# Kernel tuning notes

Hardware: AMD Instinct MI355X
Metric: run time of the kernel (lower is better)

The kernel has to match this reference:

```python
import jax, jax.numpy as jnp
import numpy as np

B, S, HID, NH, NKV, HD, PS = 4, 1024, 4096, 32, 8, 128, 16
PPS = S // PS            # pages per sequence
NP = B * PPS             # total pages
NNZ = B * S


def _llama31_freqs(head_dim):
    # flashinfer apply_llama31_rope defaults: theta=5e5, scale=8, low=1, high=4, old_ctx=8192
    half = head_dim // 2
    theta, scale, low_ff, high_ff, old_ctx = 500000.0, 8.0, 1.0, 4.0, 8192.0
    freq = 1.0 / (theta ** (jnp.arange(half, dtype=jnp.float32) * 2.0 / head_dim))
    wavelen = 2.0 * jnp.pi / freq
    low_wl, high_wl = old_ctx / low_ff, old_ctx / high_ff
    smooth = (old_ctx / wavelen - low_ff) / (high_ff - low_ff)
    return jnp.where(wavelen < high_wl, freq,
                     jnp.where(wavelen > low_wl, freq / scale,
                               (1.0 - smooth) * freq / scale + smooth * freq))


def _rope(x, pos, freqs):
    # x: [nnz, H, D], non-interleaved (rotate-half) layout
    ang = pos.astype(jnp.float32)[:, None] * freqs[None, :]          # [nnz, D/2]
    cos, sin = jnp.cos(ang)[:, None, :], jnp.sin(ang)[:, None, :]    # [nnz, 1, D/2]
    x1, x2 = jnp.split(x, 2, axis=-1)
    return jnp.concatenate([x1 * cos - x2 * sin, x2 * cos + x1 * sin], axis=-1)


def setup_inputs() -> dict:
    key = jax.random.key(0)
    ks = jax.random.split(key, 6)
    std = 0.02
    return {
        "hidden_states": jax.random.normal(ks[0], (NNZ, HID), jnp.float32),
        "wq": jax.random.normal(ks[1], (NH * HD, HID), jnp.float32) * std,
        "wk": jax.random.normal(ks[2], (NKV * HD, HID), jnp.float32) * std,
        "wv": jax.random.normal(ks[3], (NKV * HD, HID), jnp.float32) * std,
        "wo": jax.random.normal(ks[4], (HID, NH * HD), jnp.float32) * std,
        "kv_cache": jnp.zeros((1, NP, 2, PS, NKV, HD), jnp.float32),
        "position_ids": jnp.tile(jnp.arange(S, dtype=jnp.int32), B),
        "kv_page_indices": jnp.arange(NP, dtype=jnp.int32),
        "kv_page_indptr": jnp.arange(B + 1, dtype=jnp.int32) * PPS,
        "kv_last_page_lens": jnp.full((B,), PS, jnp.int32),
        "qo_indptr": jnp.arange(B + 1, dtype=jnp.int32) * S,
    }


def reference(hidden_states, wq, wk, wv, wo, kv_cache, position_ids,
              kv_page_indices, kv_page_indptr, kv_last_page_lens, qo_indptr):
    nnz = hidden_states.shape[0]
    b = qo_indptr.shape[0] - 1
    s = nnz // b
    # fused QKV projections (nn.Linear stores [out, in])
    q = (hidden_states @ wq.T).reshape(nnz, NH, HD)
    k = (hidden_states @ wk.T).reshape(nnz, NKV, HD)
    v = (hidden_states @ wv.T).reshape(nnz, NKV, HD)
    # inline Llama-3.1 RoPE with per-token position ids
    freqs = _llama31_freqs(HD)
    q = _rope(q, position_ids, freqs)
    k = _rope(k, position_ids, freqs)
    # paged-KV append: scatter k/v into pages at (page_id, slot)
    cache = kv_cache[0]                                   # [NP, 2, PS, NKV, HD]
    ps = cache.shape[2]
    pages = kv_page_indices.reshape(b, -1)                # [B, PPS]
    bidx = jnp.repeat(jnp.arange(b), s)
    pid = pages[bidx, position_ids // ps]
    slot = position_ids % ps
    cache = cache.at[pid, 0, slot].set(k).at[pid, 1, slot].set(v)
    # paged attention: gather per-sequence K/V from pages, causal SDPA with GQA
    flat = pages.reshape(-1)
    kf = cache[flat, 0].reshape(b, s, NKV, HD)
    vf = cache[flat, 1].reshape(b, s, NKV, HD)
    g = NH // NKV
    kr = jnp.repeat(kf, g, axis=2)                        # [B, S, NH, HD]
    vr = jnp.repeat(vf, g, axis=2)
    qb = q.reshape(b, s, NH, HD)
    scale = 1.0 / jnp.sqrt(jnp.float32(HD))
    scores = jnp.einsum('bqhd,bkhd->bhqk', qb, kr) * scale
    mask = jnp.tril(jnp.ones((s, s), bool))
    scores = jnp.where(mask[None, None], scores, jnp.float32(-1e30))
    attn = jax.nn.softmax(scores, axis=-1)
    out = jnp.einsum('bhqk,bkhd->bqhd', attn, vr).reshape(nnz, NH * HD)
    return out @ wo.T
```

## Files before the change

### kernel.cpp

```cpp
#include <hip/hip_runtime.h>

typedef unsigned short u16;
typedef __bf16 bf16x8 __attribute__((ext_vector_type(8)));
typedef float f32x4 __attribute__((ext_vector_type(4)));

__device__ __forceinline__ u16 f2bf(float f) {
  unsigned int u = __float_as_uint(f);
  u += 0x7fffu + ((u >> 16) & 1u);
  return (u16)(u >> 16);
}
__device__ __forceinline__ float bf2f(u16 v) {
  return __uint_as_float(((unsigned int)v) << 16);
}

__device__ __forceinline__ void gl_lds16(const u16* g, u16* l) {
  auto* lp = reinterpret_cast<__attribute__((address_space(3))) unsigned int*>(
      reinterpret_cast<uintptr_t>(l));
  auto* gp = reinterpret_cast<const __attribute__((address_space(1))) unsigned int*>(
      reinterpret_cast<uintptr_t>(g));
  __builtin_amdgcn_global_load_lds(gp, lp, 16, 0, 0);
}

__global__ __launch_bounds__(256) void cvt_kernel(const float* __restrict__ in,
                                                  u16* __restrict__ out, int n4) {
  int i = blockIdx.x * 256 + threadIdx.x;
  if (i >= n4) return;
  float4 v = ((const float4*)in)[i];
  ushort4 o;
  o.x = f2bf(v.x); o.y = f2bf(v.y); o.z = f2bf(v.z); o.w = f2bf(v.w);
  ((ushort4*)out)[i] = o;
}


#define BARRIER() __builtin_amdgcn_s_barrier()
#define VMCNT(n_) asm volatile("s_waitcnt vmcnt(" #n_ ")" ::: "memory")
#define PH_SYNC()                                           \
  do {                                                      \
    BARRIER();                                              \
    asm volatile("s_waitcnt lgkmcnt(0)" ::: "memory");      \
    __builtin_amdgcn_sched_barrier(0);                      \
  } while (0)

#define STAGE_A(b_, h_, kt_)                                                        \
  gl_lds16(gA + (size_t)((h_) * 128) * K + (size_t)(kt_) * 32,                      \
           lds + (b_) * 16384 + (h_) * 4096 + w * 512)

#define STAGE_B(b_, h_, kt_)                                                        \
  gl_lds16(gB + (size_t)((h_) * 128) * K + (size_t)(kt_) * 32,                      \
           lds + (b_) * 16384 + 8192 + (h_) * 4096 + w * 512)

#define LOADS_A(b_, qm_)                                                            \
  do {                                                                              \
    _Pragma("unroll") for (int i2 = 0; i2 < 4; i2++)                                \
      ar[i2] = *(const bf16x8*)&lds[(b_) * 16384 + arow + ((qm_)*4 + i2) * 512 + ax]; \
  } while (0)

#define LOADS_B(b_, qn_)                                                            \
  do {                                                                              \
    _Pragma("unroll") for (int j2 = 0; j2 < 2; j2++)                                \
      br[(qn_)*2 + j2] =                                                            \
          *(const bf16x8*)&lds[(b_) * 16384 + brow + ((qn_)*2 + j2) * 512 + ax];    \
  } while (0)

#define MFMA_Q(qm_, qn_)                                                            \
  do {                                                                              \
    __builtin_amdgcn_s_setprio(1);                                                  \
    _Pragma("unroll") for (int i2 = 0; i2 < 4; i2++) {                              \
      _Pragma("unroll") for (int j2 = 0; j2 < 2; j2++) {                            \
        acc[(qm_)*4 + i2][(qn_)*2 + j2] = __builtin_amdgcn_mfma_f32_16x16x32_bf16(  \
            ar[i2], br[(qn_)*2 + j2], acc[(qm_)*4 + i2][(qn_)*2 + j2], 0, 0, 0);    \
      }                                                                             \
    }                                                                               \
    __builtin_amdgcn_s_setprio(0);                                                  \
  } while (0)

template <int OUT_BF16>
__global__ __launch_bounds__(512, 2) void gemm8p(const u16* __restrict__ A,
                                                 const u16* __restrict__ B,
                                                 void* __restrict__ Cv,
                                                 int M, int N, int K) {
  __shared__ u16 lds[32768];
  (void)M;
  const int t = threadIdx.x, lane = t & 63, w = t >> 6;
  const int col = lane & 15, quad = lane >> 4;
  const int wm = w >> 2, wn = w & 3;

  const int nwg = gridDim.x * gridDim.y;
  const int wgid = blockIdx.y * gridDim.x + blockIdx.x;
  const int xcd = wgid & 7, lin = wgid >> 3;
  const int q8 = nwg >> 3, r8 = nwg & 7;
  const int nid = (xcd < r8 ? xcd * (q8 + 1) : r8 * (q8 + 1) + (xcd - r8) * q8) + lin;
  const int m0 = (nid / gridDim.x) * 256;
  const int n0 = (nid % gridDim.x) * 256;

  const int pr_ = t >> 3;
  const int s_ = (t & 7) ^ (pr_ & 7);
  const int srow = (pr_ << 1) | (s_ >> 2);
  const int sj = s_ & 3;
  const u16* gA = A + (size_t)(m0 + srow) * K + sj * 8;
  const u16* gB = B + (size_t)(n0 + srow) * K + sj * 8;

  const int arow = wm * 4096;
  const int brow = 8192 + wn * 2048;
  const int ax = (col >> 1) * 64 +
                 (((((col & 1) << 2) | quad) ^ (col >> 1)) << 3);

  f32x4 acc[8][4] = {};
  bf16x8 ar[4], br[4];

  STAGE_A(0, 0, 0); STAGE_A(0, 1, 0);
  STAGE_B(0, 0, 0); STAGE_B(0, 1, 0);
  STAGE_B(1, 0, 1); STAGE_B(1, 1, 1);
  VMCNT(2);
  BARRIER();

  const int NIT = K >> 6;
  for (int it = 0; it < NIT - 1; ++it) {
    const int kt = it * 2;
    LOADS_A(0, 0); LOADS_B(0, 0);
    STAGE_A(1, 0, kt + 1);
    PH_SYNC(); MFMA_Q(0, 0); BARRIER();
    LOADS_B(0, 1);
    STAGE_A(1, 1, kt + 1);
    PH_SYNC(); MFMA_Q(0, 1); BARRIER();
    LOADS_A(0, 1);
    STAGE_B(0, 0, kt + 2);
    PH_SYNC(); MFMA_Q(1, 0); BARRIER();
    STAGE_B(0, 1, kt + 2);
    PH_SYNC(); MFMA_Q(1, 1); VMCNT(2); BARRIER();
    LOADS_A(1, 0); LOADS_B(1, 0);
    STAGE_A(0, 0, kt + 2);
    PH_SYNC(); MFMA_Q(0, 0); BARRIER();
    LOADS_B(1, 1);
    STAGE_A(0, 1, kt + 2);
    PH_SYNC(); MFMA_Q(0, 1); BARRIER();
    LOADS_A(1, 1);
    STAGE_B(1, 0, kt + 3);
    PH_SYNC(); MFMA_Q(1, 0); BARRIER();
    STAGE_B(1, 1, kt + 3);
    PH_SYNC(); MFMA_Q(1, 1); VMCNT(2); BARRIER();
  }

  {
    const int kl = 2 * NIT - 1;
    LOADS_A(0, 0); LOADS_B(0, 0);
    STAGE_A(1, 0, kl);
    PH_SYNC(); MFMA_Q(0, 0); BARRIER();
    LOADS_B(0, 1);
    STAGE_A(1, 1, kl);
    PH_SYNC(); MFMA_Q(0, 1); BARRIER();
    LOADS_A(0, 1);
    PH_SYNC(); MFMA_Q(1, 0); BARRIER();
    PH_SYNC(); MFMA_Q(1, 1); VMCNT(0); BARRIER();
    LOADS_A(1, 0); LOADS_B(1, 0);
    PH_SYNC(); MFMA_Q(0, 0); BARRIER();
    LOADS_B(1, 1);
    PH_SYNC(); MFMA_Q(0, 1); BARRIER();
    LOADS_A(1, 1);
    PH_SYNC(); MFMA_Q(1, 0); BARRIER();
    MFMA_Q(1, 1);
  }

#pragma unroll
  for (int i = 0; i < 8; i++) {
#pragma unroll
    for (int j = 0; j < 4; j++) {
      const int mb = m0 + wm * 128 + i * 16 + quad * 4;
      const int n = n0 + wn * 64 + j * 16 + col;
#pragma unroll
      for (int r = 0; r < 4; r++) {
        float v = acc[i][j][r];
        if constexpr (OUT_BF16)
          ((u16*)Cv)[(size_t)(mb + r) * N + n] = f2bf(v);
        else
          ((float*)Cv)[(size_t)(mb + r) * N + n] = v;
      }
    }
  }
}

__global__ __launch_bounds__(256) void transpose_kernel(const u16* __restrict__ in,
                                                        u16* __restrict__ out,
                                                        int in_stride, int out_stride) {
  __shared__ u16 tile[64][72];
  const int t = threadIdx.x;
  const int bm = blockIdx.y;
  const int bn = blockIdx.x;
  const int r = t >> 3, c = (t & 7) * 8;
  const u16* src = in + (size_t)(bm * 64 + r) * in_stride + bn * 64 + c;
  *(uint4*)&tile[r][c] = *(const uint4*)src;
  *(uint4*)&tile[r + 32][c] = *(const uint4*)(src + (size_t)32 * in_stride);
  __syncthreads();
  u16 vals[8];
  u16* dst = out + (size_t)(bn * 64 + r) * out_stride + bm * 64 + c;
#pragma unroll
  for (int i = 0; i < 8; i++) vals[i] = tile[c + i][r];
  *(uint4*)dst = *(uint4*)vals;
#pragma unroll
  for (int i = 0; i < 8; i++) vals[i] = tile[c + i][r + 32];
  *(uint4*)(dst + (size_t)32 * out_stride) = *(uint4*)vals;
}

__global__ __launch_bounds__(256) void rope_kernel(u16* __restrict__ X,
                                                   const int* __restrict__ pos_ids,
                                                   int log2H, int row_stride) {
  int tid = blockIdx.x * 256 + threadIdx.x;
  int i = tid & 63;
  int rest = tid >> 6;
  int h = rest & ((1 << log2H) - 1);
  int token = rest >> log2H;
  float pos = (float)pos_ids[token];
  float fr = __builtin_exp2f(-(float)i * (18.93156856932417f / 64.0f));
  float wl = 6.283185307179586f / fr;
  float f2;
  if (wl < 2048.0f) f2 = fr;
  else if (wl > 8192.0f) f2 = fr * 0.125f;
  else {
    float sm = (8192.0f / wl - 1.0f) * (1.0f / 3.0f);
    f2 = (1.0f - sm) * fr * 0.125f + sm * fr;
  }
  float ang = pos * f2;
  float ss = sinf(ang), cc = cosf(ang);
  size_t base = (size_t)token * row_stride + (size_t)h * 128 + i;
  float x1 = bf2f(X[base]), x2 = bf2f(X[base + 64]);
  X[base] = f2bf(x1 * cc - x2 * ss);
  X[base + 64] = f2bf(x2 * cc + x1 * ss);
}

__global__ __launch_bounds__(256) void attn_kernel(const u16* __restrict__ Qg,
                                                   const u16* __restrict__ Kg,
                                                   const u16* __restrict__ VTg,
                                                   u16* __restrict__ Og,
                                                   int QS, int KS) {
  const int qt = 15 - blockIdx.x;
  const int h = blockIdx.y, b = blockIdx.z;
  const int kvh = h >> 2;
  const int t = threadIdx.x, lane = t & 63, w = t >> 6;
  const int col = lane & 15, quad = lane >> 4;

  __shared__ u16 Ks[2][64 * 128];
  __shared__ u16 Vt[2][128 * 64];
  __shared__ u16 Ps[4][16][72];

  const u16* Kbase = Kg + (size_t)(b * 1024) * KS + kvh * 128;
  const u16* Vbase = VTg + (size_t)(kvh * 128) * 4096 + b * 1024;

  auto stage_kv = [&](int bb, int j) {
#pragma unroll
    for (int c = 0; c < 4; c++) {
      int ch = w * 4 + c;
      int krow = ch * 4 + (lane >> 4);
      int kg = (lane & 15) ^ (krow & 15);
      gl_lds16(Kbase + (size_t)(j * 64 + krow) * KS + kg * 8, &Ks[bb][ch * 512]);
      int vrow = ch * 8 + (lane >> 3);
      int vg = (lane & 7) ^ (vrow & 7);
      gl_lds16(Vbase + (size_t)vrow * 4096 + j * 64 + vg * 8, &Vt[bb][ch * 512]);
    }
  };

  {
    const u16* Qbase = Qg + (size_t)(b * 1024 + qt * 64) * QS + h * 128;
#pragma unroll
    for (int c = 0; c < 4; c++) {
      int ch = w * 4 + c;
      int row = ch * 4 + (lane >> 4);
      int g = (lane & 15) ^ (row & 15);
      gl_lds16(Qbase + (size_t)row * QS + g * 8, &Ks[0][ch * 512]);
    }
  }
  stage_kv(1, 0);
  __syncthreads();
  bf16x8 qa[4];
#pragma unroll
  for (int kk = 0; kk < 4; kk++) {
    int row = w * 16 + col;
    qa[kk] = *(const bf16x8*)&Ks[0][row * 128 + (((quad + 4 * kk) ^ col) << 3)];
  }
  BARRIER();

  f32x4 o[8] = {};
  float m_i[4] = {-3.0e38f, -3.0e38f, -3.0e38f, -3.0e38f};
  float l_i[4] = {};

  const float cf = 0.08838834764831845f * 1.4426950408889634f;
  const int qrow0 = qt * 64 + w * 16 + quad * 4;

  for (int j = 0; j <= qt; j++) {
    const int bb = (j + 1) & 1;
    if (j < qt) {
      stage_kv(bb ^ 1, j + 1);
      VMCNT(8);
    } else {
      VMCNT(0);
    }
    BARRIER();

    const u16* Ksb = &Ks[bb][0];
    const u16* Vtb = &Vt[bb][0];

    f32x4 s[4] = {};
    __builtin_amdgcn_s_setprio(1);
#pragma unroll
    for (int nb = 0; nb < 4; nb++) {
      int key = nb * 16 + col;
#pragma unroll
      for (int kk = 0; kk < 4; kk++) {
        bf16x8 kb2 = *(const bf16x8*)&Ksb[key * 128 + (((quad + 4 * kk) ^ col) << 3)];
        s[nb] = __builtin_amdgcn_mfma_f32_16x16x32_bf16(qa[kk], kb2, s[nb], 0, 0, 0);
      }
    }
    __builtin_amdgcn_s_setprio(0);

    if (j == qt) {
#pragma unroll
      for (int nb = 0; nb < 4; nb++)
#pragma unroll
        for (int rr = 0; rr < 4; rr++)
          if (j * 64 + nb * 16 + col > qrow0 + rr) s[nb][rr] = -3.0e38f;
    }

    float mnew[4];
#pragma unroll
    for (int rr = 0; rr < 4; rr++) {
      mnew[rr] = m_i[rr];
#pragma unroll
      for (int nb = 0; nb < 4; nb++) mnew[rr] = fmaxf(mnew[rr], s[nb][rr]);
    }
#pragma unroll
    for (int off = 1; off < 16; off <<= 1)
#pragma unroll
      for (int rr = 0; rr < 4; rr++)
        mnew[rr] = fmaxf(mnew[rr], __shfl_xor(mnew[rr], off));

    float p[4][4], rs[4], alpha[4];
#pragma unroll
    for (int rr = 0; rr < 4; rr++) {
      alpha[rr] = __builtin_exp2f((m_i[rr] - mnew[rr]) * cf);
      m_i[rr] = mnew[rr];
      rs[rr] = 0.0f;
    }
#pragma unroll
    for (int nb = 0; nb < 4; nb++)
#pragma unroll
      for (int rr = 0; rr < 4; rr++) {
        p[nb][rr] = __builtin_exp2f((s[nb][rr] - mnew[rr]) * cf);
        rs[rr] += p[nb][rr];
      }
#pragma unroll
    for (int off = 1; off < 16; off <<= 1)
#pragma unroll
      for (int rr = 0; rr < 4; rr++) rs[rr] += __shfl_xor(rs[rr], off);
#pragma unroll
    for (int rr = 0; rr < 4; rr++) l_i[rr] = l_i[rr] * alpha[rr] + rs[rr];
#pragma unroll
    for (int nb2 = 0; nb2 < 8; nb2++)
#pragma unroll
      for (int rr = 0; rr < 4; rr++) o[nb2][rr] *= alpha[rr];

#pragma unroll
    for (int nb = 0; nb < 4; nb++)
#pragma unroll
      for (int rr = 0; rr < 4; rr++)
        Ps[w][quad * 4 + rr][nb * 16 + col] = f2bf(p[nb][rr]);

    bf16x8 pa0 = *(const bf16x8*)&Ps[w][col][quad * 8];
    bf16x8 pa1 = *(const bf16x8*)&Ps[w][col][quad * 8 + 32];
    __builtin_amdgcn_s_setprio(1);
#pragma unroll
    for (int nb2 = 0; nb2 < 8; nb2++) {
      int d = nb2 * 16 + col;
      bf16x8 vb0 = *(const bf16x8*)&Vtb[d * 64 + ((quad ^ (col & 7)) << 3)];
      bf16x8 vb1 = *(const bf16x8*)&Vtb[d * 64 + ((((quad + 4) & 7) ^ (col & 7)) << 3)];
      o[nb2] = __builtin_amdgcn_mfma_f32_16x16x32_bf16(pa0, vb0, o[nb2], 0, 0, 0);
      o[nb2] = __builtin_amdgcn_mfma_f32_16x16x32_bf16(pa1, vb1, o[nb2], 0, 0, 0);
    }
    __builtin_amdgcn_s_setprio(0);

    BARRIER();
  }

  float inv[4];
#pragma unroll
  for (int rr = 0; rr < 4; rr++) inv[rr] = 1.0f / l_i[rr];
#pragma unroll
  for (int nb2 = 0; nb2 < 8; nb2++)
#pragma unroll
    for (int rr = 0; rr < 4; rr++) {
      size_t off2 = (size_t)(b * 1024 + qt * 64 + w * 16 + quad * 4 + rr) * 4096 +
                    h * 128 + nb2 * 16 + col;
      Og[off2] = f2bf(o[nb2][rr] * inv[rr]);
    }
}

extern "C" void kernel_launch(void* const* d_in, const int* in_sizes, int n_in,
                              void* d_out, int out_size, void* d_ws, size_t ws_size,
                              hipStream_t stream) {
  const float* hs = (const float*)d_in[0];
  const float* wq = (const float*)d_in[1];
  const float* wk = (const float*)d_in[2];
  const float* wv = (const float*)d_in[3];
  const float* wo = (const float*)d_in[4];
  const int* pos = (const int*)d_in[6];
  float* out = (float*)d_out;

  char* ws = (char*)d_ws;
  const size_t MB = 1ull << 20;
  u16* hs_bf   = (u16*)(ws + 0);
  u16* wqkv_bf = (u16*)(ws + 32 * MB);
  u16* QKV     = (u16*)(ws + 80 * MB);
  u16* wo_bf = (u16*)(ws + 0);
  u16* AOb   = (u16*)(ws + 32 * MB);
  u16* VTb   = (u16*)(ws + 64 * MB);

  cvt_kernel<<<16384, 256, 0, stream>>>(hs, hs_bf, 4194304);
  cvt_kernel<<<16384, 256, 0, stream>>>(wq, wqkv_bf, 4194304);
  cvt_kernel<<<4096, 256, 0, stream>>>(wk, wqkv_bf + 16777216, 1048576);
  cvt_kernel<<<4096, 256, 0, stream>>>(wv, wqkv_bf + 20971520, 1048576);

  gemm8p<1><<<dim3(24, 16), 512, 0, stream>>>(hs_bf, wqkv_bf, QKV, 4096, 6144, 4096);

  rope_kernel<<<32768, 256, 0, stream>>>(QKV, pos, 5, 6144);
  rope_kernel<<<8192, 256, 0, stream>>>(QKV + 4096, pos, 3, 6144);

  transpose_kernel<<<dim3(16, 64), 256, 0, stream>>>(QKV + 5120, VTb, 6144, 4096);

  cvt_kernel<<<16384, 256, 0, stream>>>(wo, wo_bf, 4194304);

  attn_kernel<<<dim3(16, 32, 4), 256, 0, stream>>>(QKV, QKV + 4096, VTb, AOb, 6144, 6144);

  gemm8p<0><<<dim3(16, 16), 512, 0, stream>>>(AOb, wo_bf, out, 4096, 4096, 4096);
}
```

Before: 801.4 us.

## Process two adjacent query tiles per attention block to reuse staged K/V

Each attention workgroup now handles two consecutive 64-row query tiles, with a separate set of accumulators for each. Every K/V tile staged into LDS is used by both query tiles, which halves K/V global loads and the number of workgroups. The causal mask is now applied on every iteration instead of only the diagonal tile. Holding two sets of accumulators raises register pressure, and launch_bounds(256,2) is added to cap it; fewer workgroups may also lower parallelism and load balance.

```diff
diff --git a/kernel.cpp b/kernel.cpp
--- a/kernel.cpp
+++ b/kernel.cpp
@@ -227,12 +227,13 @@
   X[base + 64] = f2bf(x2 * cc + x1 * ss);
 }
 
-__global__ __launch_bounds__(256) void attn_kernel(const u16* __restrict__ Qg,
-                                                   const u16* __restrict__ Kg,
-                                                   const u16* __restrict__ VTg,
-                                                   u16* __restrict__ Og,
-                                                   int QS, int KS) {
-  const int qt = 15 - blockIdx.x;
+__global__ __launch_bounds__(256, 2) void attn_kernel(const u16* __restrict__ Qg,
+                                                      const u16* __restrict__ Kg,
+                                                      const u16* __restrict__ VTg,
+                                                      u16* __restrict__ Og,
+                                                      int QS, int KS) {
+  const int qtp = 7 - blockIdx.x;
+  const int qA = qtp * 2, qB = qA + 1;
   const int h = blockIdx.y, b = blockIdx.z;
   const int kvh = h >> 2;
   const int t = threadIdx.x, lane = t & 63, w = t >> 6;
@@ -259,45 +260,40 @@
   };
 
   {
-    const u16* Qbase = Qg + (size_t)(b * 1024 + qt * 64) * QS + h * 128;
+    const u16* QbA = Qg + (size_t)(b * 1024 + qA * 64) * QS + h * 128;
+    const u16* QbB = Qg + (size_t)(b * 1024 + qB * 64) * QS + h * 128;
 #pragma unroll
     for (int c = 0; c < 4; c++) {
       int ch = w * 4 + c;
       int row = ch * 4 + (lane >> 4);
       int g = (lane & 15) ^ (row & 15);
-      gl_lds16(Qbase + (size_t)row * QS + g * 8, &Ks[0][ch * 512]);
+      gl_lds16(QbA + (size_t)row * QS + g * 8, &Ks[0][ch * 512]);
+      gl_lds16(QbB + (size_t)row * QS + g * 8, &Vt[0][ch * 512]);
     }
   }
   stage_kv(1, 0);
   __syncthreads();
-  bf16x8 qa[4];
+  bf16x8 qaA[4], qaB[4];
 #pragma unroll
   for (int kk = 0; kk < 4; kk++) {
     int row = w * 16 + col;
-    qa[kk] = *(const bf16x8*)&Ks[0][row * 128 + (((quad + 4 * kk) ^ col) << 3)];
+    int off = row * 128 + (((quad + 4 * kk) ^ col) << 3);
+    qaA[kk] = *(const bf16x8*)&Ks[0][off];
+    qaB[kk] = *(const bf16x8*)&Vt[0][off];
   }
   BARRIER();
 
-  f32x4 o[8] = {};
-  float m_i[4] = {-3.0e38f, -3.0e38f, -3.0e38f, -3.0e38f};
-  float l_i[4] = {};
+  f32x4 oA[8] = {}, oB[8] = {};
+  float mA[4] = {-3.0e38f, -3.0e38f, -3.0e38f, -3.0e38f};
+  float mB[4] = {-3.0e38f, -3.0e38f, -3.0e38f, -3.0e38f};
+  float lA[4] = {}, lB[4] = {};
 
   const float cf = 0.08838834764831845f * 1.4426950408889634f;
-  const int qrow0 = qt * 64 + w * 16 + quad * 4;
-
-  for (int j = 0; j <= qt; j++) {
-    const int bb = (j + 1) & 1;
-    if (j < qt) {
-      stage_kv(bb ^ 1, j + 1);
-      VMCNT(8);
-    } else {
-      VMCNT(0);
-    }
-    BARRIER();
-
-    const u16* Ksb = &Ks[bb][0];
-    const u16* Vtb = &Vt[bb][0];
-
+  const int qr0A = qA * 64 + w * 16 + quad * 4;
+  const int qr0B = qB * 64 + w * 16 + quad * 4;
+
+  auto process = [&](const u16* Ksb, const u16* Vtb, int j, bf16x8 (&qa)[4],
+                     f32x4 (&o)[8], float (&m_i)[4], float (&l_i)[4], int qrow0) {
     f32x4 s[4] = {};
     __builtin_amdgcn_s_setprio(1);
 #pragma unroll
@@ -311,13 +307,11 @@
     }
     __builtin_amdgcn_s_setprio(0);
 
-    if (j == qt) {
-#pragma unroll
-      for (int nb = 0; nb < 4; nb++)
-#pragma unroll
-        for (int rr = 0; rr < 4; rr++)
-          if (j * 64 + nb * 16 + col > qrow0 + rr) s[nb][rr] = -3.0e38f;
-    }
+#pragma unroll
+    for (int nb = 0; nb < 4; nb++)
+#pragma unroll
+      for (int rr = 0; rr < 4; rr++)
+        if (j * 64 + nb * 16 + col > qrow0 + rr) s[nb][rr] = -3.0e38f;
 
     float mnew[4];
 #pragma unroll
@@ -375,21 +369,41 @@
       o[nb2] = __builtin_amdgcn_mfma_f32_16x16x32_bf16(pa1, vb1, o[nb2], 0, 0, 0);
     }
     __builtin_amdgcn_s_setprio(0);
-
+  };
+
+  for (int j = 0; j <= qB; j++) {
+    const int bb = (j + 1) & 1;
+    if (j < qB) {
+      stage_kv(bb ^ 1, j + 1);
+      VMCNT(8);
+    } else {
+      VMCNT(0);
+    }
     BARRIER();
-  }
-
-  float inv[4];
-#pragma unroll
-  for (int rr = 0; rr < 4; rr++) inv[rr] = 1.0f / l_i[rr];
-#pragma unroll
-  for (int nb2 = 0; nb2 < 8; nb2++)
-#pragma unroll
-    for (int rr = 0; rr < 4; rr++) {
-      size_t off2 = (size_t)(b * 1024 + qt * 64 + w * 16 + quad * 4 + rr) * 4096 +
+
+    const u16* Ksb = &Ks[bb][0];
+    const u16* Vtb = &Vt[bb][0];
+
+    if (j <= qA) process(Ksb, Vtb, j, qaA, oA, mA, lA, qr0A);
+    process(Ksb, Vtb, j, qaB, oB, mB, lB, qr0B);
+
+    BARRIER();
+  }
+
+#pragma unroll
+  for (int rr = 0; rr < 4; rr++) {
+    float invA = 1.0f / lA[rr];
+    float invB = 1.0f / lB[rr];
+#pragma unroll
+    for (int nb2 = 0; nb2 < 8; nb2++) {
+      size_t offA = (size_t)(b * 1024 + qA * 64 + w * 16 + quad * 4 + rr) * 4096 +
                     h * 128 + nb2 * 16 + col;
-      Og[off2] = f2bf(o[nb2][rr] * inv[rr]);
-    }
+      size_t offB = (size_t)(b * 1024 + qB * 64 + w * 16 + quad * 4 + rr) * 4096 +
+                    h * 128 + nb2 * 16 + col;
+      Og[offA] = f2bf(oA[nb2][rr] * invA);
+      Og[offB] = f2bf(oB[nb2][rr] * invB);
+    }
+  }
 }
 
 extern "C" void kernel_launch(void* const* d_in, const int* in_sizes, int n_in,
@@ -426,7 +440,7 @@
 
   cvt_kernel<<<16384, 256, 0, stream>>>(wo, wo_bf, 4194304);
 
-  attn_kernel<<<dim3(16, 32, 4), 256, 0, stream>>>(QKV, QKV + 4096, VTb, AOb, 6144, 6144);
+  attn_kernel<<<dim3(8, 32, 4), 256, 0, stream>>>(QKV, QKV + 4096, VTb, AOb, 6144, 6144);
 
   gemm8p<0><<<dim3(16, 16), 512, 0, stream>>>(AOb, wo_bf, out, 4096, 4096, 4096);
 }
```

Measured after the change: 784.6 us. 1.02x faster.
